# Kernel optimization log

Measured on AMD Instinct MI355X. Metric: run time of the kernel, lower is better.

The kernel has to match this reference:

```python
import jax, jax.numpy as jnp
import numpy as np

B, S, E, H = 4, 2048, 1024, 16
D = E // H  # head dim = 64

def setup_inputs() -> dict:
    key = jax.random.key(0)
    k1, k2, k3 = jax.random.split(key, 3)
    scale = 0.02
    return {
        "x": jax.random.normal(k1, (B, S, E), dtype=jnp.float32),
        "W_qkv": jax.random.normal(k2, (E, 3 * E), dtype=jnp.float32) * scale,
        "b_qkv": jnp.zeros((3 * E,), dtype=jnp.float32),
        "W_o": jax.random.normal(k3, (E, E), dtype=jnp.float32) * scale,
        "b_o": jnp.zeros((E,), dtype=jnp.float32),
    }

def reference(x, W_qkv, b_qkv, W_o, b_o):
    # dropout is identity in eval mode
    qkv = x @ W_qkv + b_qkv                      # [B, S, 3E]
    q, k, v = jnp.split(qkv, 3, axis=-1)          # each [B, S, E]
    def split_heads(t):
        return t.reshape(B, S, H, D).transpose(0, 2, 1, 3)  # [B, H, S, D]
    q, k, v = split_heads(q), split_heads(k), split_heads(v)
    scores = jnp.einsum("bhsd,bhtd->bhst", q, k) / jnp.sqrt(jnp.float32(D))
    causal = jnp.tril(jnp.ones((S, S), dtype=bool))
    scores = jnp.where(causal[None, None], scores, jnp.float32(-jnp.inf))
    attn = jax.nn.softmax(scores, axis=-1)        # [B, H, S, S]
    out = jnp.einsum("bhst,bhtd->bhsd", attn, v)  # [B, H, S, D]
    out = out.transpose(0, 2, 1, 3).reshape(B, S, E)
    return out @ W_o + b_o
```

## Files before the change

### kernel.cpp

```cpp
#include <hip/hip_runtime.h>
#include <stdint.h>

typedef __bf16 bf16_t;
typedef __bf16 bf16x8 __attribute__((ext_vector_type(8)));
typedef float f32x4 __attribute__((ext_vector_type(4)));

#define LOG2E 1.44269504088896340736f

__device__ __forceinline__ float fexp2(float x) {
#if __has_builtin(__builtin_amdgcn_exp2f)
    return __builtin_amdgcn_exp2f(x);
#else
    return exp2f(x);
#endif
}

__device__ __forceinline__ void gld_lds16(const bf16_t* g, bf16_t* l) {
    __builtin_amdgcn_global_load_lds(
        (__attribute__((address_space(1))) void*)(bf16_t*)g,
        (__attribute__((address_space(3))) void*)l,
        16, 0, 0);
}

__global__ __launch_bounds__(256) void prep_k(
    const float* __restrict__ x, bf16_t* __restrict__ xb,
    const float* __restrict__ Wqkv, bf16_t* __restrict__ wqkvT,
    const float* __restrict__ Wo, bf16_t* __restrict__ woT)
{
    const int tid = threadIdx.x;
    int blk = blockIdx.x;
    if (blk < 2048) {
        const size_t base = (size_t)blk * 4096 + tid * 4;
        #pragma unroll
        for (int it = 0; it < 4; ++it) {
            const size_t i = base + (size_t)it * 1024;
            float4 v = *(const float4*)(x + i);
            union { bf16_t b[4]; uint2 u; } u;
            u.b[0] = (bf16_t)v.x; u.b[1] = (bf16_t)v.y;
            u.b[2] = (bf16_t)v.z; u.b[3] = (bf16_t)v.w;
            *(uint2*)(xb + i) = u.u;
        }
        return;
    }
    __shared__ float t[32][33];
    const float* in; bf16_t* out; int C, tiles_x, ti;
    if (blk < 2816) { blk -= 2048; in = Wqkv; out = wqkvT; C = 3072; tiles_x = 96; ti = blk * 4; }
    else            { blk -= 2816; in = Wo;   out = woT;   C = 1024; tiles_x = 32; ti = blk * 4; }
    const int R = 1024;
    const int tx = tid & 31, ty = tid >> 5;
    const int oc = tid >> 3, rg = (tid & 7) * 4;
    for (int tt = 0; tt < 4; ++tt, ++ti) {
        const int bx = ti % tiles_x, by = ti / tiles_x;
        const int c0 = bx * 32, r0 = by * 32;
        __syncthreads();
        #pragma unroll
        for (int j = 0; j < 32; j += 8)
            t[ty + j][tx] = in[(size_t)(r0 + ty + j) * C + c0 + tx];
        __syncthreads();
        union { bf16_t b[4]; uint2 u; } u;
        u.b[0] = (bf16_t)t[rg][oc];
        u.b[1] = (bf16_t)t[rg + 1][oc];
        u.b[2] = (bf16_t)t[rg + 2][oc];
        u.b[3] = (bf16_t)t[rg + 3][oc];
        *(uint2*)(out + (size_t)(c0 + oc) * R + r0 + rg) = u.u;
    }
}

__device__ __forceinline__ void gemm_body_pipe(
    const bf16_t* __restrict__ A, const bf16_t* __restrict__ Bt,
    bf16_t* Al, bf16_t* Bl, f32x4 (&acc)[4][4], int m0, int n0)
{
    const int tid = threadIdx.x;
    const int w = tid >> 6, lane = tid & 63;
    const int l15 = lane & 15, quad = lane >> 4;
    const int wm = w >> 2, wn = w & 3;

    const int srow = lane >> 3;
    const int scg = ((lane & 7) ^ srow) * 8;
    const bf16_t* Ag = A  + (size_t)(m0 + w * 16 + srow) * 1024 + scg;
    const bf16_t* Bg = Bt + (size_t)(n0 + w * 32 + srow) * 1024 + scg;

    const int rc0 = (quad ^ (l15 & 7)) * 8;
    const int rc1 = ((quad + 4) ^ (l15 & 7)) * 8;

    auto stage0 = [&](int kt, int ss) {
        gld_lds16(Ag + kt * 64,                       Al + ss * 8192  + (w * 16) * 64);
        gld_lds16(Ag + kt * 64 + (size_t)8 * 1024,    Al + ss * 8192  + (w * 16 + 8) * 64);
        gld_lds16(Bg + kt * 64,                       Bl + ss * 16384 + (w * 32) * 64);
    };
    auto stage1 = [&](int kt, int ss) {
        gld_lds16(Bg + kt * 64 + (size_t)8 * 1024,    Bl + ss * 16384 + (w * 32 + 8) * 64);
        gld_lds16(Bg + kt * 64 + (size_t)16 * 1024,   Bl + ss * 16384 + (w * 32 + 16) * 64);
        gld_lds16(Bg + kt * 64 + (size_t)24 * 1024,   Bl + ss * 16384 + (w * 32 + 24) * 64);
    };

    stage0(0, 0); stage1(0, 0);
    stage0(1, 1); stage1(1, 1);
    asm volatile("s_waitcnt vmcnt(6)" ::: "memory");
    __builtin_amdgcn_s_barrier();

    int cs = 0, ss = 2;
    for (int t = 0; t < 16; ++t) {
        const bf16_t* Ab = Al + cs * 8192;
        const bf16_t* Bb = Bl + cs * 16384;
        {
            bf16x8 af[4], bfr[4];
            #pragma unroll
            for (int mi = 0; mi < 4; mi++)
                af[mi] = *(const bf16x8*)(Ab + (wm * 64 + mi * 16 + l15) * 64 + rc0);
            #pragma unroll
            for (int ni = 0; ni < 4; ni++)
                bfr[ni] = *(const bf16x8*)(Bb + (wn * 64 + ni * 16 + l15) * 64 + rc0);
            if (t < 14) stage0(t + 2, ss);
            __builtin_amdgcn_s_barrier();
            __builtin_amdgcn_s_setprio(1);
            #pragma unroll
            for (int mi = 0; mi < 4; mi++)
                #pragma unroll
                for (int ni = 0; ni < 4; ni++)
                    acc[mi][ni] = __builtin_amdgcn_mfma_f32_16x16x32_bf16(
                        af[mi], bfr[ni], acc[mi][ni], 0, 0, 0);
            __builtin_amdgcn_s_setprio(0);
            __builtin_amdgcn_s_barrier();
        }
        {
            bf16x8 af[4], bfr[4];
            #pragma unroll
            for (int mi = 0; mi < 4; mi++)
                af[mi] = *(const bf16x8*)(Ab + (wm * 64 + mi * 16 + l15) * 64 + rc1);
            #pragma unroll
            for (int ni = 0; ni < 4; ni++)
                bfr[ni] = *(const bf16x8*)(Bb + (wn * 64 + ni * 16 + l15) * 64 + rc1);
            if (t < 14) {
                stage1(t + 2, ss);
                asm volatile("s_waitcnt vmcnt(6)" ::: "memory");
            } else if (t == 14) {
                asm volatile("s_waitcnt vmcnt(0)" ::: "memory");
            }
            __builtin_amdgcn_s_barrier();
            __builtin_amdgcn_s_setprio(1);
            #pragma unroll
            for (int mi = 0; mi < 4; mi++)
                #pragma unroll
                for (int ni = 0; ni < 4; ni++)
                    acc[mi][ni] = __builtin_amdgcn_mfma_f32_16x16x32_bf16(
                        af[mi], bfr[ni], acc[mi][ni], 0, 0, 0);
            __builtin_amdgcn_s_setprio(0);
            __builtin_amdgcn_s_barrier();
        }
        cs = (cs == 2) ? 0 : cs + 1;
        ss = (ss == 2) ? 0 : ss + 1;
    }
}

__global__ __launch_bounds__(512) void gemm_qkv_k(
    const bf16_t* __restrict__ X, const bf16_t* __restrict__ WT,
    const float* __restrict__ bias,
    bf16_t* __restrict__ Qb, bf16_t* __restrict__ Kb, bf16_t* __restrict__ VTb)
{
    __shared__ bf16_t Al[3 * 128 * 64];
    __shared__ bf16_t Bl[3 * 256 * 64];
    const int tid = threadIdx.x;
    const int lane = tid & 63, w = tid >> 6;
    const int l15 = lane & 15, quad = lane >> 4;
    const int wm = w >> 2, wn = w & 3;

    const int wg = blockIdx.x + (blockIdx.y << 5);
    const int xcd = wg & 7, slot = wg >> 3;
    const int bx = xcd * 4 + (slot & 3);
    const int by = slot >> 2;
    const int n0 = bx * 256;
    const int m0 = by * 128;

    f32x4 acc[4][4];
    #pragma unroll
    for (int mi = 0; mi < 4; mi++)
        #pragma unroll
        for (int ni = 0; ni < 4; ni++) acc[mi][ni] = (f32x4){0.f, 0.f, 0.f, 0.f};

    gemm_body_pipe(WT, X, Al, Bl, acc, m0, n0);

    const float QSCALE = 0.125f * LOG2E;
    const int region = m0 >> 10;
    #pragma unroll
    for (int mi = 0; mi < 4; mi++) {
        const int mbase = m0 + wm * 64 + mi * 16 + quad * 4;
        const float4 bia = *(const float4*)(bias + mbase);
        const float ba[4] = {bia.x, bia.y, bia.z, bia.w};
        const int col = mbase & 1023;
        const int h = col >> 6, dbase = col & 63;
        #pragma unroll
        for (int ni = 0; ni < 4; ni++) {
            const int n = n0 + wn * 64 + ni * 16 + l15;
            const int b = n >> 11, s = n & 2047;
            if (region == 0) {
                union { bf16_t bv[4]; uint2 u; } u;
                #pragma unroll
                for (int r = 0; r < 4; r++)
                    u.bv[r] = (bf16_t)((acc[mi][ni][r] + ba[r]) * QSCALE);
                *(uint2*)(Qb + (((size_t)b * 16 + h) * 2048 + s) * 64 + dbase) = u.u;
            } else if (region == 1) {
                union { bf16_t bv[4]; uint2 u; } u;
                #pragma unroll
                for (int r = 0; r < 4; r++)
                    u.bv[r] = (bf16_t)(acc[mi][ni][r] + ba[r]);
                *(uint2*)(Kb + (((size_t)b * 16 + h) * 2048 + s) * 64 + dbase) = u.u;
            } else {
                bf16_t* dst = VTb + (((size_t)b * 16 + h) * 64 + dbase) * 2048 + s;
                #pragma unroll
                for (int r = 0; r < 4; r++)
                    dst[(size_t)r * 2048] = (bf16_t)(acc[mi][ni][r] + ba[r]);
            }
        }
    }
}

__global__ __launch_bounds__(256) void attn_k(
    const bf16_t* __restrict__ Qb, const bf16_t* __restrict__ Kb,
    const bf16_t* __restrict__ VTb, bf16_t* __restrict__ Ob)
{
    __shared__ bf16_t Kl[2][64 * 64];
    __shared__ bf16_t Vl[2][64 * 64];
    __shared__ bf16_t Pl[4][32 * 72];

    const int tid = threadIdx.x;
    const int w = tid >> 6, lane = tid & 63;
    const int l15 = lane & 15, quad = lane >> 4;
    const int idx = blockIdx.x;
    const int qt = 15 - (idx >> 6);
    const int bh = idx & 63;
    const int b = bh >> 4, h = bh & 15;
    const int q0 = qt * 128;

    const bf16_t* Qp = Qb + (size_t)bh * 2048 * 64;
    const bf16_t* Kp = Kb + (size_t)bh * 2048 * 64;
    const bf16_t* Vp = VTb + (size_t)bh * 64 * 2048;

    const int srow = w * 16 + (lane >> 3);
    const int scol = ((lane & 7) ^ ((lane >> 3) & 7)) * 8;
    const int rc0 = (quad ^ (l15 & 7)) * 8;
    const int rc1 = ((quad + 4) ^ (l15 & 7)) * 8;

    bf16x8 aq[2][2];
    #pragma unroll
    for (int g = 0; g < 2; g++) {
        const int qrow = q0 + w * 32 + g * 16 + l15;
        aq[g][0] = *(const bf16x8*)(Qp + (size_t)qrow * 64 + quad * 8);
        aq[g][1] = *(const bf16x8*)(Qp + (size_t)qrow * 64 + 32 + quad * 8);
    }

    bf16x8 vone;
    #pragma unroll
    for (int j = 0; j < 8; j++) vone[j] = (bf16_t)1.0f;

    f32x4 o[2][4];
    #pragma unroll
    for (int g = 0; g < 2; g++)
        #pragma unroll
        for (int ni = 0; ni < 4; ni++) o[g][ni] = (f32x4){0.f, 0.f, 0.f, 0.f};
    f32x4 lacc[2];
    lacc[0] = (f32x4){0.f, 0.f, 0.f, 0.f};
    lacc[1] = (f32x4){0.f, 0.f, 0.f, 0.f};

    const int nkv = (q0 >> 6) + 2;

    auto stage = [&](int kvt, int buf) {
        const int kv0 = kvt << 6;
        gld_lds16(Kp + (size_t)(kv0 + srow) * 64 + scol, Kl[buf] + (w * 16) * 64);
        gld_lds16(Kp + (size_t)(kv0 + srow + 8) * 64 + scol, Kl[buf] + (w * 16 + 8) * 64);
        gld_lds16(Vp + (size_t)srow * 2048 + kv0 + scol, Vl[buf] + (w * 16) * 64);
        gld_lds16(Vp + (size_t)(srow + 8) * 2048 + kv0 + scol, Vl[buf] + (w * 16 + 8) * 64);
    };

    stage(0, 0);

    for (int t = 0; t < nkv; ++t) {
        const int buf = t & 1;
        const int kv0 = t << 6;
        __builtin_amdgcn_s_barrier();
        if (t + 1 < nkv) {
            stage(t + 1, buf ^ 1);
            asm volatile("s_waitcnt vmcnt(4)" ::: "memory");
        } else {
            asm volatile("s_waitcnt vmcnt(0)" ::: "memory");
        }
        __builtin_amdgcn_s_barrier();

        const bf16_t* Kb_ = Kl[buf];
        const bf16_t* Vb_ = Vl[buf];

        bf16x8 ak[4][2], bv[4][2];
        #pragma unroll
        for (int ni = 0; ni < 4; ni++) {
            ak[ni][0] = *(const bf16x8*)(Kb_ + (ni * 16 + l15) * 64 + rc0);
            ak[ni][1] = *(const bf16x8*)(Kb_ + (ni * 16 + l15) * 64 + rc1);
        }
        #pragma unroll
        for (int ni = 0; ni < 4; ni++) {
            bv[ni][0] = *(const bf16x8*)(Vb_ + (ni * 16 + l15) * 64 + rc0);
            bv[ni][1] = *(const bf16x8*)(Vb_ + (ni * 16 + l15) * 64 + rc1);
        }

        #pragma unroll
        for (int g = 0; g < 2; g++) {
            const int qloc = w * 32 + g * 16 + l15;
            f32x4 sv[4];
            #pragma unroll
            for (int ni = 0; ni < 4; ni++) {
                f32x4 z = (f32x4){0.f, 0.f, 0.f, 0.f};
                z = __builtin_amdgcn_mfma_f32_16x16x32_bf16(ak[ni][0], aq[g][0], z, 0, 0, 0);
                z = __builtin_amdgcn_mfma_f32_16x16x32_bf16(ak[ni][1], aq[g][1], z, 0, 0, 0);
                sv[ni] = z;
            }

            if (kv0 >= q0) {
                const int koff = kv0 - q0;
                #pragma unroll
                for (int ni = 0; ni < 4; ni++)
                    #pragma unroll
                    for (int r = 0; r < 4; r++)
                        if (koff + ni * 16 + quad * 4 + r > qloc) sv[ni][r] = -INFINITY;
            }

            #pragma unroll
            for (int ni = 0; ni < 4; ni++) {
                union { bf16_t bvv[4]; uint2 u; } pk;
                #pragma unroll
                for (int r = 0; r < 4; r++) pk.bvv[r] = (bf16_t)fexp2(sv[ni][r]);
                *(uint2*)(&Pl[w][(g * 16 + l15) * 72 + ni * 16 + quad * 4]) = pk.u;
            }

            bf16x8 pa0 = *(const bf16x8*)(&Pl[w][(g * 16 + l15) * 72 + quad * 8]);
            bf16x8 pa1 = *(const bf16x8*)(&Pl[w][(g * 16 + l15) * 72 + 32 + quad * 8]);
            #pragma unroll
            for (int ni = 0; ni < 4; ni++) {
                o[g][ni] = __builtin_amdgcn_mfma_f32_16x16x32_bf16(bv[ni][0], pa0, o[g][ni], 0, 0, 0);
                o[g][ni] = __builtin_amdgcn_mfma_f32_16x16x32_bf16(bv[ni][1], pa1, o[g][ni], 0, 0, 0);
            }
            lacc[g] = __builtin_amdgcn_mfma_f32_16x16x32_bf16(vone, pa0, lacc[g], 0, 0, 0);
            lacc[g] = __builtin_amdgcn_mfma_f32_16x16x32_bf16(vone, pa1, lacc[g], 0, 0, 0);
        }
    }

    #pragma unroll
    for (int g = 0; g < 2; g++) {
        const float inv = 1.0f / lacc[g][0];
        const int s = q0 + w * 32 + g * 16 + l15;
        bf16_t* obase = Ob + ((size_t)b * 2048 + s) * 1024 + h * 64;
        #pragma unroll
        for (int ni = 0; ni < 4; ni++) {
            union { bf16_t bvv[4]; uint2 u; } u;
            #pragma unroll
            for (int r = 0; r < 4; r++) u.bvv[r] = (bf16_t)(o[g][ni][r] * inv);
            *(uint2*)(obase + ni * 16 + quad * 4) = u.u;
        }
    }
}

__global__ __launch_bounds__(512) void gemm_out_k(
    const bf16_t* __restrict__ O, const bf16_t* __restrict__ WT,
    const float* __restrict__ bias, float* __restrict__ out)
{
    __shared__ bf16_t Al[3 * 128 * 64];
    __shared__ bf16_t Bl[3 * 256 * 64];
    const int tid = threadIdx.x;
    const int lane = tid & 63, w = tid >> 6;
    const int l15 = lane & 15, quad = lane >> 4;
    const int wm = w >> 2, wn = w & 3;

    const int wg = blockIdx.x + (blockIdx.y << 5);
    const int xcd = wg & 7, slot = wg >> 3;
    const int bx = xcd * 4 + (slot & 3);
    const int by = slot >> 2;
    const int n0 = bx * 256;
    const int m0 = by * 128;

    f32x4 acc[4][4];
    #pragma unroll
    for (int mi = 0; mi < 4; mi++)
        #pragma unroll
        for (int ni = 0; ni < 4; ni++) acc[mi][ni] = (f32x4){0.f, 0.f, 0.f, 0.f};

    gemm_body_pipe(WT, O, Al, Bl, acc, m0, n0);

    #pragma unroll
    for (int mi = 0; mi < 4; mi++) {
        const int mbase = m0 + wm * 64 + mi * 16 + quad * 4;
        const float4 bia = *(const float4*)(bias + mbase);
        #pragma unroll
        for (int ni = 0; ni < 4; ni++) {
            const int n = n0 + wn * 64 + ni * 16 + l15;
            float4 v;
            v.x = acc[mi][ni][0] + bia.x;
            v.y = acc[mi][ni][1] + bia.y;
            v.z = acc[mi][ni][2] + bia.z;
            v.w = acc[mi][ni][3] + bia.w;
            *(float4*)(out + (size_t)n * 1024 + mbase) = v;
        }
    }
}


extern "C" void kernel_launch(void* const* d_in, const int* in_sizes, int n_in,
                              void* d_out, int out_size, void* d_ws, size_t ws_size,
                              hipStream_t stream) {
    const float* x     = (const float*)d_in[0];
    const float* W_qkv = (const float*)d_in[1];
    const float* b_qkv = (const float*)d_in[2];
    const float* W_o   = (const float*)d_in[3];
    const float* b_o   = (const float*)d_in[4];
    float* out = (float*)d_out;

    char* ws = (char*)d_ws;
    size_t off = 0;
    auto alloc = [&](size_t bytes) -> void* {
        void* p = ws + off;
        off += (bytes + 255) & ~(size_t)255;
        return p;
    };
    bf16_t* xb    = (bf16_t*)alloc((size_t)8192 * 1024 * 2);
    bf16_t* wqkvT = (bf16_t*)alloc((size_t)3072 * 1024 * 2);
    bf16_t* woT   = (bf16_t*)alloc((size_t)1024 * 1024 * 2);
    bf16_t* Qb    = (bf16_t*)alloc((size_t)8192 * 1024 * 2);
    bf16_t* Kb    = (bf16_t*)alloc((size_t)8192 * 1024 * 2);
    bf16_t* VTb   = (bf16_t*)alloc((size_t)8192 * 1024 * 2);
    bf16_t* Ob    = xb;

    prep_k<<<3072, 256, 0, stream>>>(x, xb, W_qkv, wqkvT, W_o, woT);
    gemm_qkv_k<<<dim3(32, 24), 512, 0, stream>>>(xb, wqkvT, b_qkv, Qb, Kb, VTb);
    attn_k<<<1024, 256, 0, stream>>>(Qb, Kb, VTb, Ob);
    gemm_out_k<<<dim3(32, 8), 512, 0, stream>>>(Ob, woT, b_o, out);
}
```

Measured before the change: 240.1 us.

## Load K and V tiles directly from global memory instead of LDS staging

Removes the double-buffered LDS staging of K and V tiles, along with the async global-to-LDS loads and the two barriers per iteration. Each wave now reads its K and V MFMA operands straight from global memory, relying on L1/L2 caching for reuse across the four waves. This drops the barrier synchronisation and LDS traffic, but the four waves fetch the same data redundantly and there is no prefetch to hide global load latency.

```diff
diff --git a/kernel.cpp b/kernel.cpp
--- a/kernel.cpp
+++ b/kernel.cpp
@@ -219,8 +219,6 @@
     const bf16_t* __restrict__ Qb, const bf16_t* __restrict__ Kb,
     const bf16_t* __restrict__ VTb, bf16_t* __restrict__ Ob)
 {
-    __shared__ bf16_t Kl[2][64 * 64];
-    __shared__ bf16_t Vl[2][64 * 64];
     __shared__ bf16_t Pl[4][32 * 72];
 
     const int tid = threadIdx.x;
@@ -236,11 +234,6 @@
     const bf16_t* Kp = Kb + (size_t)bh * 2048 * 64;
     const bf16_t* Vp = VTb + (size_t)bh * 64 * 2048;
 
-    const int srow = w * 16 + (lane >> 3);
-    const int scol = ((lane & 7) ^ ((lane >> 3) & 7)) * 8;
-    const int rc0 = (quad ^ (l15 & 7)) * 8;
-    const int rc1 = ((quad + 4) ^ (l15 & 7)) * 8;
-
     bf16x8 aq[2][2];
     #pragma unroll
     for (int g = 0; g < 2; g++) {
@@ -264,41 +257,21 @@
 
     const int nkv = (q0 >> 6) + 2;
 
-    auto stage = [&](int kvt, int buf) {
-        const int kv0 = kvt << 6;
-        gld_lds16(Kp + (size_t)(kv0 + srow) * 64 + scol, Kl[buf] + (w * 16) * 64);
-        gld_lds16(Kp + (size_t)(kv0 + srow + 8) * 64 + scol, Kl[buf] + (w * 16 + 8) * 64);
-        gld_lds16(Vp + (size_t)srow * 2048 + kv0 + scol, Vl[buf] + (w * 16) * 64);
-        gld_lds16(Vp + (size_t)(srow + 8) * 2048 + kv0 + scol, Vl[buf] + (w * 16 + 8) * 64);
-    };
-
-    stage(0, 0);
-
     for (int t = 0; t < nkv; ++t) {
-        const int buf = t & 1;
         const int kv0 = t << 6;
-        __builtin_amdgcn_s_barrier();
-        if (t + 1 < nkv) {
-            stage(t + 1, buf ^ 1);
-            asm volatile("s_waitcnt vmcnt(4)" ::: "memory");
-        } else {
-            asm volatile("s_waitcnt vmcnt(0)" ::: "memory");
-        }
-        __builtin_amdgcn_s_barrier();
-
-        const bf16_t* Kb_ = Kl[buf];
-        const bf16_t* Vb_ = Vl[buf];
 
         bf16x8 ak[4][2], bv[4][2];
         #pragma unroll
         for (int ni = 0; ni < 4; ni++) {
-            ak[ni][0] = *(const bf16x8*)(Kb_ + (ni * 16 + l15) * 64 + rc0);
-            ak[ni][1] = *(const bf16x8*)(Kb_ + (ni * 16 + l15) * 64 + rc1);
+            const bf16_t* kr = Kp + (size_t)(kv0 + ni * 16 + l15) * 64;
+            ak[ni][0] = *(const bf16x8*)(kr + quad * 8);
+            ak[ni][1] = *(const bf16x8*)(kr + 32 + quad * 8);
         }
         #pragma unroll
         for (int ni = 0; ni < 4; ni++) {
-            bv[ni][0] = *(const bf16x8*)(Vb_ + (ni * 16 + l15) * 64 + rc0);
-            bv[ni][1] = *(const bf16x8*)(Vb_ + (ni * 16 + l15) * 64 + rc1);
+            const bf16_t* vr = Vp + (size_t)(ni * 16 + l15) * 2048 + kv0;
+            bv[ni][0] = *(const bf16x8*)(vr + quad * 8);
+            bv[ni][1] = *(const bf16x8*)(vr + 32 + quad * 8);
         }
 
         #pragma unroll
```

New measurement: 307.1 us. 1.28x slower.
